# Kernel optimization log

Hardware: AMD Instinct MI355X
Metric: run time of the kernel (lower is better)

## Reference

```python
import jax, jax.numpy as jnp
import numpy as np

IMG_H = 448
IMG_W = 448
NEG = jnp.float32(-1e30)


def make_anchors(h, w, stride, size):
    # centers at (x*stride, y*stride), single scale, ratio 1; row-major (y, x) order
    ys = jnp.arange(h, dtype=jnp.float32) * stride
    xs = jnp.arange(w, dtype=jnp.float32) * stride
    cy, cx = jnp.meshgrid(ys, xs, indexing='ij')
    cx, cy = cx.reshape(-1), cy.reshape(-1)
    half = 0.5 * size
    return jnp.stack([cx - half, cy - half, cx + half, cy + half], axis=1)  # [h*w, 4]


def iou_one_vs_all(box, boxes):
    x1 = jnp.maximum(box[0], boxes[:, 0]); y1 = jnp.maximum(box[1], boxes[:, 1])
    x2 = jnp.minimum(box[2], boxes[:, 2]); y2 = jnp.minimum(box[3], boxes[:, 3])
    inter = jnp.maximum(x2 - x1, 0.) * jnp.maximum(y2 - y1, 0.)
    a1 = (box[2] - box[0]) * (box[3] - box[1])
    a2 = (boxes[:, 2] - boxes[:, 0]) * (boxes[:, 3] - boxes[:, 1])
    return inter / (a1 + a2 - inter)


def nms_topk(anchors, scores, valid, iou_thr, topk):
    # greedy NMS: invalid (<= mean) boxes get -inf score so they are never selected
    s0 = jnp.where(valid, scores, NEG)

    def body(k, carry):
        s, out = carry
        idx = jnp.argmax(s)
        box = anchors[idx]
        sup = iou_one_vs_all(box, anchors) > iou_thr
        s = jnp.where(sup, NEG, s).at[idx].set(NEG)
        out = out.at[k].set(box)
        return (s, out)

    _, out = jax.lax.fori_loop(0, topk, body, (s0, jnp.zeros((topk, 4), jnp.float32)))
    return out  # [topk, 4]


def get_att_roi(att, stride, size, iou_thr, topk):
    n, _, h, w = att.shape
    corner = jnp.zeros((h, w), att.dtype).at[int(0.1 * h):int(0.9 * h), int(0.1 * w):int(0.9 * w)].set(1.0)
    scores = (att[:, 0] * corner).reshape(n, -1)
    valid = scores > scores.mean(axis=1, keepdims=True)  # score threshold = per-sample mean
    anchors = make_anchors(h, w, float(stride), float(size))
    boxes = jax.vmap(lambda s, v: nms_topk(anchors, s, v, iou_thr, topk))(scores, valid)  # [n, topk, 4]
    boxes = jnp.stack([
        jnp.maximum(boxes[..., 0], 0.),
        jnp.maximum(boxes[..., 1], 0.),
        jnp.minimum(boxes[..., 2], IMG_W - 1.),
        jnp.minimum(boxes[..., 3], IMG_H - 1.),
    ], axis=-1)
    ids = jnp.broadcast_to(jnp.arange(n, dtype=jnp.float32)[:, None, None], (n, topk, 1))
    return jnp.concatenate([ids, boxes], axis=-1).reshape(n * topk, 5)


def crop_resize(xi, x1i, y1i, cw, ch):
    # bilinear resize of integer crop xi[:, y1i:y1i+ch, x1i:x1i+cw] to full (H, W),
    # align_corners=False (matches F.interpolate)
    C, H, W = xi.shape

    def axis_idx(n_out, start, clen):
        s = jnp.maximum((jnp.arange(n_out, dtype=jnp.float32) + 0.5) * (clen.astype(jnp.float32) / n_out) - 0.5, 0.)
        i0 = jnp.floor(s).astype(jnp.int32)
        i1 = jnp.minimum(i0 + 1, clen - 1)
        return start + i0, start + i1, s - i0

    gy0, gy1, fy = axis_idx(H, y1i, ch)
    gx0, gx1, fx = axis_idx(W, x1i, cw)
    x00 = xi[:, gy0[:, None], gx0[None, :]]
    x01 = xi[:, gy0[:, None], gx1[None, :]]
    x10 = xi[:, gy1[:, None], gx0[None, :]]
    x11 = xi[:, gy1[:, None], gx1[None, :]]
    top = x00 + fx[None, None, :] * (x01 - x00)
    bot = x10 + fx[None, None, :] * (x11 - x10)
    return top + fy[None, :, None] * (bot - top)


def forward(x2, x3, x4, x5):
    m3 = x3.mean(1, keepdims=True)
    m4 = x4.mean(1, keepdims=True)
    m5 = x5.mean(1, keepdims=True)
    roi3 = jax.lax.stop_gradient(get_att_roi(m3, 2 ** 3, 64, 0.05, 5))
    roi4 = jax.lax.stop_gradient(get_att_roi(m4, 2 ** 4, 128, 0.05, 3))
    roi5 = jax.lax.stop_gradient(get_att_roi(m5, 2 ** 5, 256, 0.05, 1))
    n = x2.shape[0]
    scale = float(2 ** 3)
    all_b = jnp.concatenate([
        roi3.reshape(n, 5, 5)[..., 1:],
        roi4.reshape(n, 3, 5)[..., 1:],
        roi5.reshape(n, 1, 5)[..., 1:],
    ], axis=1) / scale  # [n, 9, 4] in x2 feature coords
    x1i = jnp.floor(all_b[..., 0].min(1)).astype(jnp.int32)
    y1i = jnp.floor(all_b[..., 1].min(1)).astype(jnp.int32)
    x2i = jnp.floor(all_b[..., 2].max(1)).astype(jnp.int32)
    y2i = jnp.floor(all_b[..., 3].max(1)).astype(jnp.int32)
    crop = jax.vmap(crop_resize)(x2, x1i, y1i, x2i - x1i, y2i - y1i)
    return roi3, roi4, roi5, crop


def setup_inputs() -> dict:
    key = jax.random.key(0)
    k2, k3, k4, k5 = jax.random.split(key, 4)
    return {
        'x2': jax.random.normal(k2, (32, 256, 56, 56), jnp.float32),
        'x3': jax.random.normal(k3, (32, 256, 56, 56), jnp.float32),
        'x4': jax.random.normal(k4, (32, 256, 28, 28), jnp.float32),
        'x5': jax.random.normal(k5, (32, 256, 14, 14), jnp.float32),
    }


def reference(x2, x3, x4, x5):
    return forward(x2, x3, x4, x5)
```

## Files before the change

### kernel.cpp

```cpp
#include <hip/hip_runtime.h>

#define NEGV (-1e30f)

template <int H, int W, int R0, int R1>
__device__ __forceinline__ void mean_body(int blk, const float* __restrict__ x,
                                          float* __restrict__ scores,
                                          float4* part) {
    constexpr int HW = H * W;
    constexpr int QUADS = HW / 4;
    const int tid = threadIdx.x;
    const int cg = tid >> 5;
    const int pl = tid & 31;
    const int q = blk * 32 + pl;

    const int b = q / QUADS;
    const int quad = q - b * QUADS;
    const float* base = x + (size_t)b * 256 * HW + (size_t)cg * 32 * HW + quad * 4;

    float4 acc = make_float4(0.f, 0.f, 0.f, 0.f);
#pragma unroll 8
    for (int c = 0; c < 32; ++c) {
        const float4 v = *reinterpret_cast<const float4*>(base + (size_t)c * HW);
        acc.x += v.x; acc.y += v.y; acc.z += v.z; acc.w += v.w;
    }
    part[tid] = acc;
    __syncthreads();

    if (tid < 32) {
        float4 s = part[pl];
#pragma unroll
        for (int g = 1; g < 8; ++g) {
            const float4 v = part[g * 32 + pl];
            s.x += v.x; s.y += v.y; s.z += v.z; s.w += v.w;
        }
        const int p0 = quad * 4;
        float r[4] = {s.x, s.y, s.z, s.w};
        float o[4];
#pragma unroll
        for (int e = 0; e < 4; ++e) {
            const int p = p0 + e;
            const int y = p / W;
            const int xx = p - y * W;
            const float val = r[e] * (1.0f / 256.0f);
            const bool in = (y >= R0) && (y < R1) && (xx >= R0) && (xx < R1);
            o[e] = in ? val : 0.0f;
        }
        *reinterpret_cast<float4*>(scores + (size_t)b * HW + p0) =
            make_float4(o[0], o[1], o[2], o[3]);
    }
}

__global__ __launch_bounds__(256) void mean_all_kernel(const float* __restrict__ x3,
                                                       const float* __restrict__ x4,
                                                       const float* __restrict__ x5,
                                                       float* __restrict__ sc3,
                                                       float* __restrict__ sc4,
                                                       float* __restrict__ sc5) {
    __shared__ float4 part[256];
    const int bid = blockIdx.x;
    if (bid < 784) {
        mean_body<56, 56, 5, 50>(bid, x3, sc3, part);
    } else if (bid < 980) {
        mean_body<28, 28, 2, 25>(bid - 784, x4, sc4, part);
    } else {
        mean_body<14, 14, 1, 12>(bid - 980, x5, sc5, part);
    }
}

template <int HW, int W, int TOPK, int ISTRIDE, int ISIZE>
__device__ __forceinline__ void nms_body(int b, const float* __restrict__ sc,
                                         float* __restrict__ o,
                                         float* rv, int* ri, float* rs) {
    constexpr int NPT = (HW + 255) / 256;
    const int tid = threadIdx.x;
    const int lane = tid & 63;
    const int wave = tid >> 6;

    float s[NPT];
    float sum = 0.f;
#pragma unroll
    for (int i = 0; i < NPT; ++i) {
        const int j = tid + 256 * i;
        const float v = (j < HW) ? sc[j] : NEGV;
        s[i] = v;
        if (j < HW) sum += v;
    }
#pragma unroll
    for (int off = 32; off > 0; off >>= 1) sum += __shfl_down(sum, off, 64);
    if (lane == 0) rs[wave] = sum;
    __syncthreads();
    const float mean = (rs[0] + rs[1] + rs[2] + rs[3]) / (float)HW;

#pragma unroll
    for (int i = 0; i < NPT; ++i) s[i] = (s[i] > mean) ? s[i] : NEGV;

    constexpr float half = 0.5f * (float)ISIZE;
    constexpr float area2 = 2.0f * (float)ISIZE * (float)ISIZE;

    for (int k = 0; k < TOPK; ++k) {
        float bv = -3.0e38f;
        int bi = 0x7fffffff;
#pragma unroll
        for (int i = 0; i < NPT; ++i) {
            if (s[i] > bv) { bv = s[i]; bi = tid + 256 * i; }
        }
#pragma unroll
        for (int off = 32; off > 0; off >>= 1) {
            const float ov = __shfl_down(bv, off, 64);
            const int oi = __shfl_down(bi, off, 64);
            if (ov > bv || (ov == bv && oi < bi)) { bv = ov; bi = oi; }
        }
        if (lane == 0) { rv[wave] = bv; ri[wave] = bi; }
        __syncthreads();
        float wv = rv[0];
        int wi = ri[0];
#pragma unroll
        for (int w = 1; w < 4; ++w) {
            const float v2 = rv[w];
            const int i2 = ri[w];
            if (v2 > wv || (v2 == wv && i2 < wi)) { wv = v2; wi = i2; }
        }
        __syncthreads();

        const int gy = wi / W;
        const int gx = wi - gy * W;
        const float bx1 = (float)gx * (float)ISTRIDE - half;
        const float by1 = (float)gy * (float)ISTRIDE - half;
        const float bx2 = (float)gx * (float)ISTRIDE + half;
        const float by2 = (float)gy * (float)ISTRIDE + half;

        if (tid == 0) {
            float* r = o + k * 5;
            r[0] = (float)b;
            r[1] = fmaxf(bx1, 0.f);
            r[2] = fmaxf(by1, 0.f);
            r[3] = fminf(bx2, 447.f);
            r[4] = fminf(by2, 447.f);
        }

#pragma unroll
        for (int i = 0; i < NPT; ++i) {
            const int j = tid + 256 * i;
            const int ay = j / W;
            const int ax = j - ay * W;
            const float acx = (float)ax * (float)ISTRIDE;
            const float acy = (float)ay * (float)ISTRIDE;
            const float ix1 = fmaxf(bx1, acx - half);
            const float iy1 = fmaxf(by1, acy - half);
            const float ix2 = fminf(bx2, acx + half);
            const float iy2 = fminf(by2, acy + half);
            const float inter = fmaxf(ix2 - ix1, 0.f) * fmaxf(iy2 - iy1, 0.f);
            const float iou = inter / (area2 - inter);
            if (iou > 0.05f || j == wi) s[i] = NEGV;
        }
    }
}

__global__ __launch_bounds__(256) void nms_kernel(const float* __restrict__ sc3,
                                                  const float* __restrict__ sc4,
                                                  const float* __restrict__ sc5,
                                                  float* __restrict__ out) {
    __shared__ float rv[4];
    __shared__ int ri[4];
    __shared__ float rs[4];
    const int blk = blockIdx.x;
    const int sid = blk >> 5;
    const int b = blk & 31;
    if (sid == 0) {
        nms_body<3136, 56, 5, 8, 64>(b, sc3 + (size_t)b * 3136, out + (size_t)b * 25, rv, ri, rs);
    } else if (sid == 1) {
        nms_body<784, 28, 3, 16, 128>(b, sc4 + (size_t)b * 784, out + 800 + (size_t)b * 15, rv, ri, rs);
    } else {
        nms_body<196, 14, 1, 32, 256>(b, sc5 + (size_t)b * 196, out + 1280 + (size_t)b * 5, rv, ri, rs);
    }
}

__global__ __launch_bounds__(256) void tables_kernel(const float* __restrict__ out,
                                                     int* __restrict__ ty0, int* __restrict__ ty1,
                                                     float* __restrict__ tfy,
                                                     int* __restrict__ tx0, int* __restrict__ tx1,
                                                     float* __restrict__ tfx) {
    __shared__ int sx1i[32], sy1i[32], scw[32], sch[32];
    const int tid = threadIdx.x;
    if (tid < 32) {
        const int b = tid;
        float x1 = 3.0e38f, y1 = 3.0e38f, x2 = -3.0e38f, y2 = -3.0e38f;
#pragma unroll
        for (int k = 0; k < 5; ++k) {
            const float* r = out + (size_t)(b * 5 + k) * 5;
            x1 = fminf(x1, r[1]); y1 = fminf(y1, r[2]);
            x2 = fmaxf(x2, r[3]); y2 = fmaxf(y2, r[4]);
        }
#pragma unroll
        for (int k = 0; k < 3; ++k) {
            const float* r = out + 800 + (size_t)(b * 3 + k) * 5;
            x1 = fminf(x1, r[1]); y1 = fminf(y1, r[2]);
            x2 = fmaxf(x2, r[3]); y2 = fmaxf(y2, r[4]);
        }
        {
            const float* r = out + 1280 + (size_t)b * 5;
            x1 = fminf(x1, r[1]); y1 = fminf(y1, r[2]);
            x2 = fmaxf(x2, r[3]); y2 = fmaxf(y2, r[4]);
        }
        const int x1i = (int)floorf(x1 * 0.125f);
        const int y1i = (int)floorf(y1 * 0.125f);
        const int x2i = (int)floorf(x2 * 0.125f);
        const int y2i = (int)floorf(y2 * 0.125f);
        sx1i[b] = x1i; sy1i[b] = y1i;
        scw[b] = x2i - x1i; sch[b] = y2i - y1i;
    }
    __syncthreads();

    for (int t = tid; t < 3584; t += 256) {
        const int b = t / 112;
        const int r = t - b * 112;
        const int axis = r / 56;
        const int o = r - axis * 56;
        if (axis == 0) {
            const int clen = sch[b];
            const int start = sy1i[b];
            const float s = fmaxf(((float)o + 0.5f) * ((float)clen / 56.0f) - 0.5f, 0.f);
            const int i0 = (int)s;
            const int i1 = min(i0 + 1, clen - 1);
            ty0[b * 56 + o] = (start + i0) * 56;
            ty1[b * 56 + o] = (start + i1) * 56;
            tfy[b * 56 + o] = s - (float)i0;
        } else {
            const int clen = scw[b];
            const int start = sx1i[b];
            const float s = fmaxf(((float)o + 0.5f) * ((float)clen / 56.0f) - 0.5f, 0.f);
            const int i0 = (int)s;
            const int i1 = min(i0 + 1, clen - 1);
            tx0[b * 56 + o] = start + i0;
            tx1[b * 56 + o] = start + i1;
            tfx[b * 56 + o] = s - (float)i0;
        }
    }
}

__global__ __launch_bounds__(448) void crop_kernel(const float* __restrict__ x2,
                                                   const int* __restrict__ ty0,
                                                   const int* __restrict__ ty1,
                                                   const float* __restrict__ tfy,
                                                   const int* __restrict__ tx0,
                                                   const int* __restrict__ tx1,
                                                   const float* __restrict__ tfx,
                                                   float* __restrict__ outc) {
    __shared__ int sy0[56], sy1[56];
    __shared__ float sfy[56];
    __shared__ int sx0[56], sx1[56];
    __shared__ float sfx[56];

    const int bc = blockIdx.x;
    const int b = bc >> 8;
    const int tid = threadIdx.x;

    if (tid < 336) {
        const int a = tid / 56;
        const int o = tid - a * 56;
        const int gi = b * 56 + o;
        switch (a) {
            case 0: sy0[o] = ty0[gi]; break;
            case 1: sy1[o] = ty1[gi]; break;
            case 2: sfy[o] = tfy[gi]; break;
            case 3: sx0[o] = tx0[gi]; break;
            case 4: sx1[o] = tx1[gi]; break;
            default: sfx[o] = tfx[gi]; break;
        }
    }
    __syncthreads();

    const int y0 = tid / 56;
    const int xx = tid - y0 * 56;
    const int gx0 = sx0[xx];
    const int gx1 = sx1[xx];
    const float fx = sfx[xx];

    const float* plane = x2 + (size_t)bc * 3136;
    float* op = outc + (size_t)bc * 3136;

#pragma unroll
    for (int i = 0; i < 7; ++i) {
        const int y = y0 + 8 * i;
        const int r0 = sy0[y];
        const int r1 = sy1[y];
        const float fy = sfy[y];
        const float v00 = plane[r0 + gx0];
        const float v01 = plane[r0 + gx1];
        const float v10 = plane[r1 + gx0];
        const float v11 = plane[r1 + gx1];
        const float top = v00 + fx * (v01 - v00);
        const float bot = v10 + fx * (v11 - v10);
        op[tid + 448 * i] = top + fy * (bot - top);
    }
}

extern "C" void kernel_launch(void* const* d_in, const int* in_sizes, int n_in,
                              void* d_out, int out_size, void* d_ws, size_t ws_size,
                              hipStream_t stream) {
    const float* x2 = (const float*)d_in[0];
    const float* x3 = (const float*)d_in[1];
    const float* x4 = (const float*)d_in[2];
    const float* x5 = (const float*)d_in[3];
    float* out = (float*)d_out;

    float* sc3 = (float*)d_ws;
    float* sc4 = sc3 + 32 * 3136;
    float* sc5 = sc4 + 32 * 784;
    int* ty0 = (int*)(sc5 + 32 * 196);
    int* ty1 = ty0 + 32 * 56;
    int* tx0 = ty1 + 32 * 56;
    int* tx1 = tx0 + 32 * 56;
    float* tfy = (float*)(tx1 + 32 * 56);
    float* tfx = tfy + 32 * 56;

    mean_all_kernel<<<1029, 256, 0, stream>>>(x3, x4, x5, sc3, sc4, sc5);
    nms_kernel<<<96, 256, 0, stream>>>(sc3, sc4, sc5, out);
    tables_kernel<<<1, 256, 0, stream>>>(out, ty0, ty1, tfy, tx0, tx1, tfx);
    crop_kernel<<<8192, 448, 0, stream>>>(x2, ty0, ty1, tfy, tx0, tx1, tfx, out + 1440);
}
```

Baseline: 291.7 us.

## Fuse NMS with crop tables using one wave per level, stage crop rows in LDS

NMS now runs one 64-lane wave per pyramid level, and a single block per sample handles all three levels. This replaces block-wide reductions and barriers with wave shuffles. The separate tables kernel is folded into that block, which computes the union box from shared memory, so one launch is removed. The crop kernel copies the needed rows of each x2 plane into LDS with float4 loads and then gathers the bilinear taps from LDS. The cost is a 12.5 KB LDS buffer per block and a serial NMS of 3136 elements on a single wave with 49 values per lane.

New measurement: 304.0 us. 1.04x slower.

```diff
diff --git a/kernel.cpp b/kernel.cpp
--- a/kernel.cpp
+++ b/kernel.cpp
@@ -67,29 +67,25 @@
     }
 }
 
-template <int HW, int W, int TOPK, int ISTRIDE, int ISIZE>
-__device__ __forceinline__ void nms_body(int b, const float* __restrict__ sc,
-                                         float* __restrict__ o,
-                                         float* rv, int* ri, float* rs) {
-    constexpr int NPT = (HW + 255) / 256;
-    const int tid = threadIdx.x;
-    const int lane = tid & 63;
-    const int wave = tid >> 6;
+template <int HW, int W, int TOPK, int ISTRIDE, int ISIZE, int BOXOFF>
+__device__ __forceinline__ void nms_wave(int b, const float* __restrict__ sc,
+                                         float* __restrict__ obox,
+                                         float (*sbox)[4]) {
+    constexpr int NPT = (HW + 63) / 64;
+    const int lane = threadIdx.x & 63;
 
     float s[NPT];
     float sum = 0.f;
 #pragma unroll
     for (int i = 0; i < NPT; ++i) {
-        const int j = tid + 256 * i;
+        const int j = lane + 64 * i;
         const float v = (j < HW) ? sc[j] : NEGV;
         s[i] = v;
         if (j < HW) sum += v;
     }
 #pragma unroll
     for (int off = 32; off > 0; off >>= 1) sum += __shfl_down(sum, off, 64);
-    if (lane == 0) rs[wave] = sum;
-    __syncthreads();
-    const float mean = (rs[0] + rs[1] + rs[2] + rs[3]) / (float)HW;
+    const float mean = __shfl(sum, 0, 64) / (float)HW;
 
 #pragma unroll
     for (int i = 0; i < NPT; ++i) s[i] = (s[i] > mean) ? s[i] : NEGV;
@@ -102,7 +98,7 @@
         int bi = 0x7fffffff;
 #pragma unroll
         for (int i = 0; i < NPT; ++i) {
-            if (s[i] > bv) { bv = s[i]; bi = tid + 256 * i; }
+            if (s[i] > bv) { bv = s[i]; bi = lane + 64 * i; }
         }
 #pragma unroll
         for (int off = 32; off > 0; off >>= 1) {
@@ -110,17 +106,7 @@
             const int oi = __shfl_down(bi, off, 64);
             if (ov > bv || (ov == bv && oi < bi)) { bv = ov; bi = oi; }
         }
-        if (lane == 0) { rv[wave] = bv; ri[wave] = bi; }
-        __syncthreads();
-        float wv = rv[0];
-        int wi = ri[0];
-#pragma unroll
-        for (int w = 1; w < 4; ++w) {
-            const float v2 = rv[w];
-            const int i2 = ri[w];
-            if (v2 > wv || (v2 == wv && i2 < wi)) { wv = v2; wi = i2; }
-        }
-        __syncthreads();
+        const int wi = __shfl(bi, 0, 64);
 
         const int gy = wi / W;
         const int gx = wi - gy * W;
@@ -129,18 +115,23 @@
         const float bx2 = (float)gx * (float)ISTRIDE + half;
         const float by2 = (float)gy * (float)ISTRIDE + half;
 
-        if (tid == 0) {
-            float* r = o + k * 5;
+        if (lane == 0) {
+            const float c0 = fmaxf(bx1, 0.f);
+            const float c1 = fmaxf(by1, 0.f);
+            const float c2 = fminf(bx2, 447.f);
+            const float c3 = fminf(by2, 447.f);
+            float* r = obox + k * 5;
             r[0] = (float)b;
-            r[1] = fmaxf(bx1, 0.f);
-            r[2] = fmaxf(by1, 0.f);
-            r[3] = fminf(bx2, 447.f);
-            r[4] = fminf(by2, 447.f);
+            r[1] = c0; r[2] = c1; r[3] = c2; r[4] = c3;
+            sbox[BOXOFF + k][0] = c0;
+            sbox[BOXOFF + k][1] = c1;
+            sbox[BOXOFF + k][2] = c2;
+            sbox[BOXOFF + k][3] = c3;
         }
 
 #pragma unroll
         for (int i = 0; i < NPT; ++i) {
-            const int j = tid + 256 * i;
+            const int j = lane + 64 * i;
             const int ay = j / W;
             const int ax = j - ay * W;
             const float acx = (float)ax * (float)ISTRIDE;
@@ -156,89 +147,76 @@
     }
 }
 
-__global__ __launch_bounds__(256) void nms_kernel(const float* __restrict__ sc3,
-                                                  const float* __restrict__ sc4,
-                                                  const float* __restrict__ sc5,
-                                                  float* __restrict__ out) {
-    __shared__ float rv[4];
-    __shared__ int ri[4];
-    __shared__ float rs[4];
-    const int blk = blockIdx.x;
-    const int sid = blk >> 5;
-    const int b = blk & 31;
-    if (sid == 0) {
-        nms_body<3136, 56, 5, 8, 64>(b, sc3 + (size_t)b * 3136, out + (size_t)b * 25, rv, ri, rs);
-    } else if (sid == 1) {
-        nms_body<784, 28, 3, 16, 128>(b, sc4 + (size_t)b * 784, out + 800 + (size_t)b * 15, rv, ri, rs);
-    } else {
-        nms_body<196, 14, 1, 32, 256>(b, sc5 + (size_t)b * 196, out + 1280 + (size_t)b * 5, rv, ri, rs);
-    }
-}
-
-__global__ __launch_bounds__(256) void tables_kernel(const float* __restrict__ out,
-                                                     int* __restrict__ ty0, int* __restrict__ ty1,
-                                                     float* __restrict__ tfy,
-                                                     int* __restrict__ tx0, int* __restrict__ tx1,
-                                                     float* __restrict__ tfx) {
-    __shared__ int sx1i[32], sy1i[32], scw[32], sch[32];
+__global__ __launch_bounds__(256) void nms_tables_kernel(const float* __restrict__ sc3,
+                                                         const float* __restrict__ sc4,
+                                                         const float* __restrict__ sc5,
+                                                         float* __restrict__ out,
+                                                         int* __restrict__ ty0, int* __restrict__ ty1,
+                                                         float* __restrict__ tfy,
+                                                         int* __restrict__ tx0, int* __restrict__ tx1,
+                                                         float* __restrict__ tfx,
+                                                         int* __restrict__ bnds) {
+    __shared__ float sbox[9][4];
+    __shared__ int sb[4];
+
+    const int b = blockIdx.x;
     const int tid = threadIdx.x;
-    if (tid < 32) {
-        const int b = tid;
+    const int wave = tid >> 6;
+
+    if (wave == 0) {
+        nms_wave<3136, 56, 5, 8, 64, 0>(b, sc3 + (size_t)b * 3136, out + (size_t)b * 25, sbox);
+    } else if (wave == 1) {
+        nms_wave<784, 28, 3, 16, 128, 5>(b, sc4 + (size_t)b * 784, out + 800 + (size_t)b * 15, sbox);
+    } else if (wave == 2) {
+        nms_wave<196, 14, 1, 32, 256, 8>(b, sc5 + (size_t)b * 196, out + 1280 + (size_t)b * 5, sbox);
+    }
+    __syncthreads();
+
+    if (tid == 0) {
         float x1 = 3.0e38f, y1 = 3.0e38f, x2 = -3.0e38f, y2 = -3.0e38f;
 #pragma unroll
-        for (int k = 0; k < 5; ++k) {
-            const float* r = out + (size_t)(b * 5 + k) * 5;
-            x1 = fminf(x1, r[1]); y1 = fminf(y1, r[2]);
-            x2 = fmaxf(x2, r[3]); y2 = fmaxf(y2, r[4]);
-        }
-#pragma unroll
-        for (int k = 0; k < 3; ++k) {
-            const float* r = out + 800 + (size_t)(b * 3 + k) * 5;
-            x1 = fminf(x1, r[1]); y1 = fminf(y1, r[2]);
-            x2 = fmaxf(x2, r[3]); y2 = fmaxf(y2, r[4]);
-        }
-        {
-            const float* r = out + 1280 + (size_t)b * 5;
-            x1 = fminf(x1, r[1]); y1 = fminf(y1, r[2]);
-            x2 = fmaxf(x2, r[3]); y2 = fmaxf(y2, r[4]);
+        for (int i = 0; i < 9; ++i) {
+            x1 = fminf(x1, sbox[i][0]);
+            y1 = fminf(y1, sbox[i][1]);
+            x2 = fmaxf(x2, sbox[i][2]);
+            y2 = fmaxf(y2, sbox[i][3]);
         }
         const int x1i = (int)floorf(x1 * 0.125f);
         const int y1i = (int)floorf(y1 * 0.125f);
         const int x2i = (int)floorf(x2 * 0.125f);
         const int y2i = (int)floorf(y2 * 0.125f);
-        sx1i[b] = x1i; sy1i[b] = y1i;
-        scw[b] = x2i - x1i; sch[b] = y2i - y1i;
+        sb[0] = x1i; sb[1] = y1i; sb[2] = x2i - x1i; sb[3] = y2i - y1i;
+        bnds[b * 2 + 0] = y1i;
+        bnds[b * 2 + 1] = y2i - y1i;
     }
     __syncthreads();
 
-    for (int t = tid; t < 3584; t += 256) {
-        const int b = t / 112;
-        const int r = t - b * 112;
-        const int axis = r / 56;
-        const int o = r - axis * 56;
+    if (tid < 112) {
+        const int axis = tid / 56;
+        const int o = tid - axis * 56;
         if (axis == 0) {
-            const int clen = sch[b];
-            const int start = sy1i[b];
-            const float s = fmaxf(((float)o + 0.5f) * ((float)clen / 56.0f) - 0.5f, 0.f);
+            const int ch = sb[3];
+            const float s = fmaxf(((float)o + 0.5f) * ((float)ch / 56.0f) - 0.5f, 0.f);
             const int i0 = (int)s;
-            const int i1 = min(i0 + 1, clen - 1);
-            ty0[b * 56 + o] = (start + i0) * 56;
-            ty1[b * 56 + o] = (start + i1) * 56;
+            const int i1 = min(i0 + 1, ch - 1);
+            ty0[b * 56 + o] = i0 * 56;
+            ty1[b * 56 + o] = i1 * 56;
             tfy[b * 56 + o] = s - (float)i0;
         } else {
-            const int clen = scw[b];
-            const int start = sx1i[b];
-            const float s = fmaxf(((float)o + 0.5f) * ((float)clen / 56.0f) - 0.5f, 0.f);
+            const int cw = sb[2];
+            const int x1i = sb[0];
+            const float s = fmaxf(((float)o + 0.5f) * ((float)cw / 56.0f) - 0.5f, 0.f);
             const int i0 = (int)s;
-            const int i1 = min(i0 + 1, clen - 1);
-            tx0[b * 56 + o] = start + i0;
-            tx1[b * 56 + o] = start + i1;
+            const int i1 = min(i0 + 1, cw - 1);
+            tx0[b * 56 + o] = x1i + i0;
+            tx1[b * 56 + o] = x1i + i1;
             tfx[b * 56 + o] = s - (float)i0;
         }
     }
 }
 
 __global__ __launch_bounds__(448) void crop_kernel(const float* __restrict__ x2,
+                                                   const int* __restrict__ bnds,
                                                    const int* __restrict__ ty0,
                                                    const int* __restrict__ ty1,
                                                    const float* __restrict__ tfy,
@@ -246,6 +224,7 @@
                                                    const int* __restrict__ tx1,
                                                    const float* __restrict__ tfx,
                                                    float* __restrict__ outc) {
+    __shared__ float sp[3136];
     __shared__ int sy0[56], sy1[56];
     __shared__ float sfy[56];
     __shared__ int sx0[56], sx1[56];
@@ -254,6 +233,9 @@
     const int bc = blockIdx.x;
     const int b = bc >> 8;
     const int tid = threadIdx.x;
+
+    const int y1i = bnds[b * 2 + 0];
+    const int ch = bnds[b * 2 + 1];
 
     if (tid < 336) {
         const int a = tid / 56;
@@ -268,6 +250,11 @@
             default: sfx[o] = tfx[gi]; break;
         }
     }
+
+    const float4* src4 = reinterpret_cast<const float4*>(x2 + (size_t)bc * 3136 + y1i * 56);
+    float4* sp4 = reinterpret_cast<float4*>(sp);
+    const int n4 = ch * 14;
+    for (int i = tid; i < n4; i += 448) sp4[i] = src4[i];
     __syncthreads();
 
     const int y0 = tid / 56;
@@ -276,7 +263,6 @@
     const int gx1 = sx1[xx];
     const float fx = sfx[xx];
 
-    const float* plane = x2 + (size_t)bc * 3136;
     float* op = outc + (size_t)bc * 3136;
 
 #pragma unroll
@@ -285,10 +271,10 @@
         const int r0 = sy0[y];
         const int r1 = sy1[y];
         const float fy = sfy[y];
-        const float v00 = plane[r0 + gx0];
-        const float v01 = plane[r0 + gx1];
-        const float v10 = plane[r1 + gx0];
-        const float v11 = plane[r1 + gx1];
+        const float v00 = sp[r0 + gx0];
+        const float v01 = sp[r0 + gx1];
+        const float v10 = sp[r1 + gx0];
+        const float v11 = sp[r1 + gx1];
         const float top = v00 + fx * (v01 - v00);
         const float bot = v10 + fx * (v11 - v10);
         op[tid + 448 * i] = top + fy * (bot - top);
@@ -313,9 +299,11 @@
     int* tx1 = tx0 + 32 * 56;
     float* tfy = (float*)(tx1 + 32 * 56);
     float* tfx = tfy + 32 * 56;
+    int* bnds = (int*)(tfx + 32 * 56);
 
     mean_all_kernel<<<1029, 256, 0, stream>>>(x3, x4, x5, sc3, sc4, sc5);
-    nms_kernel<<<96, 256, 0, stream>>>(sc3, sc4, sc5, out);
-    tables_kernel<<<1, 256, 0, stream>>>(out, ty0, ty1, tfy, tx0, tx1, tfx);
-    crop_kernel<<<8192, 448, 0, stream>>>(x2, ty0, ty1, tfy, tx0, tx1, tfx, out + 1440);
-}
+    nms_tables_kernel<<<32, 256, 0, stream>>>(sc3, sc4, sc5, out,
+                                              ty0, ty1, tfy, tx0, tx1, tfx, bnds);
+    crop_kernel<<<8192, 448, 0, stream>>>(x2, bnds, ty0, ty1, tfy, tx0, tx1, tfx,
+                                          out + 1440);
+}
```
